# Kernel tuning notes

Hardware: AMD Instinct MI355X
Metric: run time of the kernel (lower is better)

## Reference

```python
import jax, jax.numpy as jnp
import numpy as np

HIDDEN_SIZE = 512  # H * d = 8 * 64


def setup_inputs() -> dict:
    key = jax.random.key(0)
    kq, kk, kv = jax.random.split(key, 3)
    B, H, S, d = 2, 8, 4096, 64
    Q = jax.random.normal(kq, (B, H, S, d), dtype=jnp.float32)
    K = jax.random.normal(kk, (B, H, d, S), dtype=jnp.float32)  # pre-transposed, as the torch module expects
    V = jax.random.normal(kv, (B, H, S, d), dtype=jnp.float32)
    return {"Q": Q, "K": K, "V": V}


def reference(Q, K, V):
    B, H, S, d = Q.shape
    scale = 1.0 / np.sqrt(HIDDEN_SIZE).astype(np.float32)
    # e: [B,H,S,S] -- full score matrix, as in the original
    e = jnp.einsum('bhsd,bhdt->bhst', Q, K) * scale
    # FAITHFUL quirk: nn.Softmax(dim=1) normalizes over the HEAD axis, not keys
    a = jax.nn.softmax(e, axis=1)
    o = jnp.einsum('bhst,bhtd->bhsd', a, V)
    # torch .view(B, S, hidden): raw contiguous reshape of [B,H,S,d]
    return o.reshape(B, S, HIDDEN_SIZE)
```

## Files before the change

### kernel.cpp

```cpp
#include <hip/hip_runtime.h>
#include <hip/hip_fp16.h>

#define S_LEN 4096
#define NHEAD 8
#define HEADD 64
#define BM 32
#define BN 32
#define TSPLIT 8
#define TCHUNK (S_LEN / TSPLIT)
#define NTILE (TCHUNK / BN)
#define EAP 48
#define KPRE 0.0637588696f

#define KT_BYTES (2ull * NHEAD * S_LEN * HEADD * 2)
#define VT_OFF   KT_BYTES
#define PART_OFF (2 * KT_BYTES)
#define PART_U32 (16ull * NHEAD * 2048 * 64)
#define WS_FULL  (PART_OFF + PART_U32 * 4)

typedef __attribute__((ext_vector_type(8))) short   short8;
typedef __attribute__((ext_vector_type(4))) float   float4v;

__device__ __forceinline__ unsigned short f2bf(float f) {
  unsigned int u = __float_as_uint(f);
  u += 0x7FFFu + ((u >> 16) & 1u);
  return (unsigned short)(u >> 16);
}
__device__ __forceinline__ float fast_exp2(float x) {
  float r; asm("v_exp_f32 %0, %1" : "=v"(r) : "v"(x)); return r;
}

__global__ __launch_bounds__(256)
void prepass_cvt(const float* __restrict__ K, const float* __restrict__ V,
                 unsigned short* __restrict__ Kt, unsigned short* __restrict__ Vt) {
  __shared__ __align__(16) unsigned short lds[64][72];
  const int tid = threadIdx.x;
  const int isV = blockIdx.x >> 10;
  const int idx = blockIdx.x & 1023;
  const int bh  = idx >> 6;
  const int t0  = (idx & 63) << 6;
  if (!isV) {
    const float* in = K + (size_t)bh * HEADD * S_LEN;
#pragma unroll
    for (int j = 0; j < 16; ++j) {
      int li = j * 256 + tid;
      int k = li >> 6, t = li & 63;
      lds[t][k] = f2bf(in[(size_t)k * S_LEN + t0 + t] * KPRE);
    }
    __syncthreads();
    unsigned short* out = Kt + (size_t)bh * S_LEN * HEADD;
    int t = tid >> 2, k0 = (tid & 3) << 4;
    *(short8*)(out + (size_t)(t0 + t) * HEADD + k0)     = *(const short8*)&lds[t][k0];
    *(short8*)(out + (size_t)(t0 + t) * HEADD + k0 + 8) = *(const short8*)&lds[t][k0 + 8];
  } else {
    const float* in = V + (size_t)bh * S_LEN * HEADD;
#pragma unroll
    for (int j = 0; j < 16; ++j) {
      int li = j * 256 + tid;
      int t = li >> 6, d = li & 63;
      lds[d][t] = f2bf(in[(size_t)(t0 + t) * HEADD + d]);
    }
    __syncthreads();
    unsigned short* out = Vt + (size_t)bh * HEADD * S_LEN;
    int d = tid >> 2, c0 = (tid & 3) << 4;
    *(short8*)(out + (size_t)d * S_LEN + t0 + c0)     = *(const short8*)&lds[d][c0];
    *(short8*)(out + (size_t)d * S_LEN + t0 + c0 + 8) = *(const short8*)&lds[d][c0 + 8];
  }
}

__global__ __launch_bounds__(512, 6)
void attn_main(const float* __restrict__ Q, const unsigned short* __restrict__ Kt,
               const unsigned short* __restrict__ Vt, unsigned int* __restrict__ part) {
  __shared__ __align__(16) unsigned short EA[2][NHEAD][BM][EAP];

  const int tid  = threadIdx.x;
  const int h    = tid >> 6;
  const int lane = tid & 63;
  const int quad = lane >> 4;
  const int l15  = lane & 15;
  const int combo = blockIdx.x & 15;
  const int b  = combo & 1;
  const int tc = combo >> 1;
  const int s0 = (blockIdx.x >> 4) * BM;

  const float* Qg = Q + (size_t)(b * NHEAD + h) * S_LEN * HEADD;
  const unsigned short* Kth = Kt + (size_t)(b * NHEAD + h) * S_LEN * HEADD;
  const unsigned short* Vth = Vt + (size_t)(b * NHEAD + h) * HEADD * S_LEN;

  short8 qf[2][2];
#pragma unroll
  for (int ss = 0; ss < 2; ++ss)
#pragma unroll
    for (int kk = 0; kk < 2; ++kk) {
      const float* p = Qg + (size_t)(s0 + ss * 16 + l15) * HEADD + kk * 32 + quad * 8;
      float4v a0 = *(const float4v*)p;
      float4v a1 = *(const float4v*)(p + 4);
      short8 f;
      f[0] = (short)f2bf(a0[0]); f[1] = (short)f2bf(a0[1]);
      f[2] = (short)f2bf(a0[2]); f[3] = (short)f2bf(a0[3]);
      f[4] = (short)f2bf(a1[0]); f[5] = (short)f2bf(a1[1]);
      f[6] = (short)f2bf(a1[2]); f[7] = (short)f2bf(a1[3]);
      qf[ss][kk] = f;
    }

  float4v acc[2][4];
#pragma unroll
  for (int ss = 0; ss < 2; ++ss)
#pragma unroll
    for (int df = 0; df < 4; ++df)
      acc[ss][df] = (float4v){0.f, 0.f, 0.f, 0.f};

  const int s_sm = tid >> 4;
  const int tp   = tid & 15;

  int t0 = tc * TCHUNK;
  for (int it = 0; it < NTILE; ++it, t0 += BN) {
    const int p = it & 1;

    {
      short8 kf[2][2];
#pragma unroll
      for (int ts = 0; ts < 2; ++ts)
#pragma unroll
        for (int kh = 0; kh < 2; ++kh)
          kf[ts][kh] = *(const short8*)(Kth + (size_t)(t0 + ts * 16 + l15) * HEADD + kh * 32 + quad * 8);
#pragma unroll
      for (int ss = 0; ss < 2; ++ss)
#pragma unroll
        for (int ts = 0; ts < 2; ++ts) {
          float4v e = (float4v){0.f, 0.f, 0.f, 0.f};
          e = __builtin_amdgcn_mfma_f32_16x16x32_bf16(qf[ss][0], kf[ts][0], e, 0, 0, 0);
          e = __builtin_amdgcn_mfma_f32_16x16x32_bf16(qf[ss][1], kf[ts][1], e, 0, 0, 0);
#pragma unroll
          for (int r = 0; r < 4; ++r)
            EA[p][h][ss * 16 + quad * 4 + r][ts * 16 + l15] =
                __half_as_ushort(__float2half(e[r]));
        }
    }
    __syncthreads();

    {
      unsigned int x[8];
#pragma unroll
      for (int hh = 0; hh < 8; ++hh)
        x[hh] = *(const unsigned int*)&EA[p][hh][s_sm][tp * 2];
      {
        float pe[8]; float sum = 0.f;
#pragma unroll
        for (int hh = 0; hh < 8; ++hh) {
          pe[hh] = fast_exp2(__half2float(__ushort_as_half((unsigned short)(x[hh] & 0xffffu))));
          sum += pe[hh];
        }
        float inv = __builtin_amdgcn_rcpf(sum);
#pragma unroll
        for (int hh = 0; hh < 8; ++hh) {
          unsigned int u = __float_as_uint(pe[hh] * inv) + 0x8000u;
          EA[p][hh][s_sm][tp * 2] = (unsigned short)(u >> 16);
        }
      }
      {
        float pe[8]; float sum = 0.f;
#pragma unroll
        for (int hh = 0; hh < 8; ++hh) {
          pe[hh] = fast_exp2(__half2float(__ushort_as_half((unsigned short)(x[hh] >> 16))));
          sum += pe[hh];
        }
        float inv = __builtin_amdgcn_rcpf(sum);
#pragma unroll
        for (int hh = 0; hh < 8; ++hh) {
          unsigned int u = __float_as_uint(pe[hh] * inv) + 0x8000u;
          EA[p][hh][s_sm][tp * 2 + 1] = (unsigned short)(u >> 16);
        }
      }
    }
    __syncthreads();

    {
      short8 vf[4];
#pragma unroll
      for (int df = 0; df < 4; ++df)
        vf[df] = *(const short8*)(Vth + (size_t)(df * 16 + l15) * S_LEN + t0 + quad * 8);
      short8 af[2];
#pragma unroll
      for (int ss = 0; ss < 2; ++ss)
        af[ss] = *(const short8*)&EA[p][h][ss * 16 + l15][quad * 8];
#pragma unroll
      for (int ss = 0; ss < 2; ++ss)
#pragma unroll
        for (int df = 0; df < 4; ++df)
          acc[ss][df] = __builtin_amdgcn_mfma_f32_16x16x32_bf16(af[ss], vf[df], acc[ss][df], 0, 0, 0);
    }
  }

  unsigned int* pb = part + ((size_t)(tc * 2 + b) * NHEAD + h) * (2048ull * 64);
  const int spb = (s0 >> 1) + quad * 2;
#pragma unroll
  for (int ss = 0; ss < 2; ++ss)
#pragma unroll
    for (int df = 0; df < 4; ++df)
#pragma unroll
      for (int rp = 0; rp < 2; ++rp) {
        unsigned int ulo = __float_as_uint(acc[ss][df][rp * 2])     + 0x8000u;
        unsigned int uhi = __float_as_uint(acc[ss][df][rp * 2 + 1]) + 0x8000u;
        unsigned int pk  = __builtin_amdgcn_perm(uhi, ulo, 0x07060302u);
        pb[(size_t)(spb + ss * 8 + rp) * 64 + df * 16 + l15] = pk;
      }
}

__global__ __launch_bounds__(256)
void reduce_partials(const unsigned int* __restrict__ part, float* __restrict__ out) {
  const size_t TCSTRIDE = 2097152;
  size_t i = ((size_t)blockIdx.x * 256 + threadIdx.x) * 4;
  if (i >= TCSTRIDE) return;
  float lo[4] = {0.f, 0.f, 0.f, 0.f}, hi[4] = {0.f, 0.f, 0.f, 0.f};
#pragma unroll
  for (int tc = 0; tc < 8; ++tc) {
    uint4 v = *(const uint4*)(part + tc * TCSTRIDE + i);
    lo[0] += __uint_as_float(v.x << 16); hi[0] += __uint_as_float(v.x & 0xffff0000u);
    lo[1] += __uint_as_float(v.y << 16); hi[1] += __uint_as_float(v.y & 0xffff0000u);
    lo[2] += __uint_as_float(v.z << 16); hi[2] += __uint_as_float(v.z & 0xffff0000u);
    lo[3] += __uint_as_float(v.w << 16); hi[3] += __uint_as_float(v.w & 0xffff0000u);
  }
  size_t bh = i >> 17;
  unsigned int r = (unsigned int)(i & 131071u);
  unsigned int sp = r >> 6, d = r & 63u;
  float* o = out + ((size_t)bh * S_LEN + 2 * sp) * HEADD + d;
  *(float4v*)o        = (float4v){lo[0], lo[1], lo[2], lo[3]};
  *(float4v*)(o + 64) = (float4v){hi[0], hi[1], hi[2], hi[3]};
}

__global__ __launch_bounds__(512, 2)
void attn_fallback(const float* __restrict__ Qg0, const float* __restrict__ Kg0,
                   const float* __restrict__ Vg0, float* __restrict__ Og0) {
  __shared__ __align__(16) unsigned short Klds[NHEAD][32][72];
  __shared__ __align__(16) unsigned short Vlds[NHEAD][HEADD][40];
  __shared__ __align__(16) unsigned short EA2[NHEAD][64][40];
  const int tid = threadIdx.x, h = tid >> 6, lane = tid & 63, quad = lane >> 4, l15 = lane & 15;
  const int b = blockIdx.x >> 6, s0 = (blockIdx.x & 63) * 64;
  const float* Qg = Qg0 + ((size_t)(b * NHEAD + h)) * S_LEN * HEADD;
  const float* Kg = Kg0 + ((size_t)(b * NHEAD + h)) * HEADD * S_LEN;
  const float* Vg = Vg0 + ((size_t)(b * NHEAD + h)) * S_LEN * HEADD;
  float* Og = Og0 + ((size_t)(b * NHEAD + h)) * S_LEN * HEADD;
  const float SC = 0.04419417382415922f;
  short8 qf[4][2];
#pragma unroll
  for (int ss = 0; ss < 4; ++ss)
#pragma unroll
    for (int kk = 0; kk < 2; ++kk) {
      const float* p = Qg + (size_t)(s0 + ss * 16 + l15) * HEADD + kk * 32 + quad * 8;
      float4v a0 = *(const float4v*)p; float4v a1 = *(const float4v*)(p + 4);
      short8 f;
      f[0] = (short)f2bf(a0[0]); f[1] = (short)f2bf(a0[1]); f[2] = (short)f2bf(a0[2]); f[3] = (short)f2bf(a0[3]);
      f[4] = (short)f2bf(a1[0]); f[5] = (short)f2bf(a1[1]); f[6] = (short)f2bf(a1[2]); f[7] = (short)f2bf(a1[3]);
      qf[ss][kk] = f;
    }
  float4v acc[4][4];
#pragma unroll
  for (int ss = 0; ss < 4; ++ss)
#pragma unroll
    for (int ds = 0; ds < 4; ++ds) acc[ss][ds] = (float4v){0.f, 0.f, 0.f, 0.f};
  const int koct = lane >> 3, kt4 = (lane & 7) * 4, vdq = lane & 15, vtg = lane >> 4;
  const int s_sm = tid >> 3, t4_sm = (tid & 7) * 4;
  for (int it = 0; it < S_LEN / 32; ++it) {
    const int t0 = it * 32;
    {
      float buf[8][4];
#pragma unroll
      for (int j = 0; j < 8; ++j) {
        float4v v = *(const float4v*)(Kg + (size_t)(koct * 8 + j) * S_LEN + t0 + kt4);
        buf[j][0] = v[0]; buf[j][1] = v[1]; buf[j][2] = v[2]; buf[j][3] = v[3];
      }
#pragma unroll
      for (int c = 0; c < 4; ++c) {
        short8 f;
#pragma unroll
        for (int j = 0; j < 8; ++j) f[j] = (short)f2bf(buf[j][c]);
        *(short8*)&Klds[h][kt4 + c][koct * 8] = f;
      }
    }
    {
      float buf[8][4];
#pragma unroll
      for (int j = 0; j < 8; ++j) {
        float4v v = *(const float4v*)(Vg + (size_t)(t0 + vtg * 8 + j) * HEADD + vdq * 4);
        buf[j][0] = v[0]; buf[j][1] = v[1]; buf[j][2] = v[2]; buf[j][3] = v[3];
      }
#pragma unroll
      for (int c = 0; c < 4; ++c) {
        short8 f;
#pragma unroll
        for (int j = 0; j < 8; ++j) f[j] = (short)f2bf(buf[j][c]);
        *(short8*)&Vlds[h][vdq * 4 + c][vtg * 8] = f;
      }
    }
    __syncthreads();
#pragma unroll
    for (int ts = 0; ts < 2; ++ts) {
      short8 kf0 = *(const short8*)&Klds[h][ts * 16 + l15][quad * 8];
      short8 kf1 = *(const short8*)&Klds[h][ts * 16 + l15][32 + quad * 8];
#pragma unroll
      for (int ss = 0; ss < 4; ++ss) {
        float4v e = (float4v){0.f, 0.f, 0.f, 0.f};
        e = __builtin_amdgcn_mfma_f32_16x16x32_bf16(qf[ss][0], kf0, e, 0, 0, 0);
        e = __builtin_amdgcn_mfma_f32_16x16x32_bf16(qf[ss][1], kf1, e, 0, 0, 0);
#pragma unroll
        for (int r = 0; r < 4; ++r)
          EA2[h][ss * 16 + quad * 4 + r][ts * 16 + l15] = __half_as_ushort(__float2half(e[r] * SC));
      }
    }
    __syncthreads();
    {
      float ev[8][4];
#pragma unroll
      for (int hh = 0; hh < 8; ++hh) {
        unsigned long long u = *(const unsigned long long*)&EA2[hh][s_sm][t4_sm];
        ev[hh][0] = __half2float(__ushort_as_half((unsigned short)u));
        ev[hh][1] = __half2float(__ushort_as_half((unsigned short)(u >> 16)));
        ev[hh][2] = __half2float(__ushort_as_half((unsigned short)(u >> 32)));
        ev[hh][3] = __half2float(__ushort_as_half((unsigned short)(u >> 48)));
      }
#pragma unroll
      for (int c = 0; c < 4; ++c) {
        float m = ev[0][c];
#pragma unroll
        for (int hh = 1; hh < 8; ++hh) m = fmaxf(m, ev[hh][c]);
        float sum = 0.f;
#pragma unroll
        for (int hh = 0; hh < 8; ++hh) { float x = __expf(ev[hh][c] - m); ev[hh][c] = x; sum += x; }
        float inv = __builtin_amdgcn_rcpf(sum);
#pragma unroll
        for (int hh = 0; hh < 8; ++hh) ev[hh][c] *= inv;
      }
#pragma unroll
      for (int hh = 0; hh < 8; ++hh) {
        unsigned short u0 = f2bf(ev[hh][0]), u1 = f2bf(ev[hh][1]), u2 = f2bf(ev[hh][2]), u3 = f2bf(ev[hh][3]);
        unsigned long long w = (unsigned long long)u0 | ((unsigned long long)u1 << 16) |
                               ((unsigned long long)u2 << 32) | ((unsigned long long)u3 << 48);
        *(unsigned long long*)&EA2[hh][s_sm][t4_sm] = w;
      }
    }
    __syncthreads();
    {
      short8 af[4], vf[4];
#pragma unroll
      for (int ss = 0; ss < 4; ++ss) af[ss] = *(const short8*)&EA2[h][ss * 16 + l15][quad * 8];
#pragma unroll
      for (int ds = 0; ds < 4; ++ds) vf[ds] = *(const short8*)&Vlds[h][ds * 16 + l15][quad * 8];
#pragma unroll
      for (int ss = 0; ss < 4; ++ss)
#pragma unroll
        for (int ds = 0; ds < 4; ++ds)
          acc[ss][ds] = __builtin_amdgcn_mfma_f32_16x16x32_bf16(af[ss], vf[ds], acc[ss][ds], 0, 0, 0);
    }
    __syncthreads();
  }
#pragma unroll
  for (int ss = 0; ss < 4; ++ss)
#pragma unroll
    for (int ds = 0; ds < 4; ++ds)
#pragma unroll
      for (int r = 0; r < 4; ++r)
        Og[(size_t)(s0 + ss * 16 + quad * 4 + r) * HEADD + ds * 16 + l15] = acc[ss][ds][r];
}

extern "C" void kernel_launch(void* const* d_in, const int* in_sizes, int n_in,
                              void* d_out, int out_size, void* d_ws, size_t ws_size,
                              hipStream_t stream) {
  const float* Q = (const float*)d_in[0];
  const float* K = (const float*)d_in[1];
  const float* V = (const float*)d_in[2];
  float* O = (float*)d_out;

  if (ws_size >= WS_FULL) {
    unsigned short* Kt = (unsigned short*)d_ws;
    unsigned short* Vt = (unsigned short*)((char*)d_ws + VT_OFF);
    unsigned int* part = (unsigned int*)((char*)d_ws + PART_OFF);
    hipLaunchKernelGGL(prepass_cvt, dim3(2048), dim3(256), 0, stream, K, V, Kt, Vt);
    hipLaunchKernelGGL(attn_main, dim3(2048), dim3(512), 0, stream, Q, Kt, Vt, part);
    hipLaunchKernelGGL(reduce_partials, dim3(2048), dim3(256), 0, stream, part, O);
  } else {
    hipLaunchKernelGGL(attn_fallback, dim3(128), dim3(512), 0, stream, Q, K, V, O);
  }
}
```

Baseline: 361.6 us.

## Fold exp into score stage and redundantly reduce head sums per warp

Each warp now applies exp2 to its own scores before writing fp16 values to LDS. After a single barrier, every warp reads all eight heads' exp values for its rows, sums them in half2, and normalizes its own head's values in registers. This removes the separate softmax pass and one __syncthreads per tile. The trade is eightfold redundant LDS reads and additions across warps, plus fp16 accumulation of the sum, which may lose precision. The LDS row padding also shrinks from 48 to 40.

```diff
diff --git a/kernel.cpp b/kernel.cpp
--- a/kernel.cpp
+++ b/kernel.cpp
@@ -1,5 +1,6 @@
 #include <hip/hip_runtime.h>
 #include <hip/hip_fp16.h>
+#include <cmath>
 
 #define S_LEN 4096
 #define NHEAD 8
@@ -9,7 +10,7 @@
 #define TSPLIT 8
 #define TCHUNK (S_LEN / TSPLIT)
 #define NTILE (TCHUNK / BN)
-#define EAP 48
+#define EAP 40
 #define KPRE 0.0637588696f
 
 #define KT_BYTES (2ull * NHEAD * S_LEN * HEADD * 2)
@@ -25,9 +26,6 @@
   unsigned int u = __float_as_uint(f);
   u += 0x7FFFu + ((u >> 16) & 1u);
   return (unsigned short)(u >> 16);
-}
-__device__ __forceinline__ float fast_exp2(float x) {
-  float r; asm("v_exp_f32 %0, %1" : "=v"(r) : "v"(x)); return r;
 }
 
 __global__ __launch_bounds__(256)
@@ -110,12 +108,11 @@
     for (int df = 0; df < 4; ++df)
       acc[ss][df] = (float4v){0.f, 0.f, 0.f, 0.f};
 
-  const int s_sm = tid >> 4;
-  const int tp   = tid & 15;
-
-  int t0 = tc * TCHUNK;
-  for (int it = 0; it < NTILE; ++it, t0 += BN) {
-    const int p = it & 1;
+  const int tbase = tc * TCHUNK;
+
+  for (int it = 0; it < NTILE; ++it) {
+    const int t0 = tbase + it * BN;
+    const int p  = it & 1;
 
     {
       short8 kf[2][2];
@@ -132,64 +129,51 @@
           e = __builtin_amdgcn_mfma_f32_16x16x32_bf16(qf[ss][0], kf[ts][0], e, 0, 0, 0);
           e = __builtin_amdgcn_mfma_f32_16x16x32_bf16(qf[ss][1], kf[ts][1], e, 0, 0, 0);
 #pragma unroll
-          for (int r = 0; r < 4; ++r)
+          for (int r = 0; r < 4; ++r) {
+            float ex = exp2f(e[r]);
             EA[p][h][ss * 16 + quad * 4 + r][ts * 16 + l15] =
-                __half_as_ushort(__float2half(e[r]));
+                __half_as_ushort(__float2half(ex));
+          }
         }
     }
     __syncthreads();
 
-    {
-      unsigned int x[8];
-#pragma unroll
-      for (int hh = 0; hh < 8; ++hh)
-        x[hh] = *(const unsigned int*)&EA[p][hh][s_sm][tp * 2];
-      {
-        float pe[8]; float sum = 0.f;
-#pragma unroll
-        for (int hh = 0; hh < 8; ++hh) {
-          pe[hh] = fast_exp2(__half2float(__ushort_as_half((unsigned short)(x[hh] & 0xffffu))));
-          sum += pe[hh];
-        }
-        float inv = __builtin_amdgcn_rcpf(sum);
-#pragma unroll
-        for (int hh = 0; hh < 8; ++hh) {
-          unsigned int u = __float_as_uint(pe[hh] * inv) + 0x8000u;
-          EA[p][hh][s_sm][tp * 2] = (unsigned short)(u >> 16);
-        }
-      }
-      {
-        float pe[8]; float sum = 0.f;
-#pragma unroll
-        for (int hh = 0; hh < 8; ++hh) {
-          pe[hh] = fast_exp2(__half2float(__ushort_as_half((unsigned short)(x[hh] >> 16))));
-          sum += pe[hh];
-        }
-        float inv = __builtin_amdgcn_rcpf(sum);
-#pragma unroll
-        for (int hh = 0; hh < 8; ++hh) {
-          unsigned int u = __float_as_uint(pe[hh] * inv) + 0x8000u;
-          EA[p][hh][s_sm][tp * 2 + 1] = (unsigned short)(u >> 16);
-        }
-      }
-    }
-    __syncthreads();
-
-    {
-      short8 vf[4];
+    short8 vf[4];
+#pragma unroll
+    for (int df = 0; df < 4; ++df)
+      vf[df] = *(const short8*)(Vth + (size_t)(df * 16 + l15) * S_LEN + t0 + quad * 8);
+
+    short8 af[2];
+#pragma unroll
+    for (int ss = 0; ss < 2; ++ss) {
+      const int row = ss * 16 + l15;
+      union { short8 s8; __half2 h2[4]; } w, own;
+      __half2 z[4];
+      w.s8 = *(const short8*)&EA[p][0][row][quad * 8];
+      z[0] = w.h2[0]; z[1] = w.h2[1]; z[2] = w.h2[2]; z[3] = w.h2[3];
+#pragma unroll
+      for (int hh = 1; hh < 8; ++hh) {
+        w.s8 = *(const short8*)&EA[p][hh][row][quad * 8];
+        z[0] = __hadd2(z[0], w.h2[0]); z[1] = __hadd2(z[1], w.h2[1]);
+        z[2] = __hadd2(z[2], w.h2[2]); z[3] = __hadd2(z[3], w.h2[3]);
+      }
+      own.s8 = *(const short8*)&EA[p][h][row][quad * 8];
+      short8 a8;
+#pragma unroll
+      for (int j = 0; j < 4; ++j) {
+        float il = __builtin_amdgcn_rcpf(__low2float(z[j]));
+        float ih = __builtin_amdgcn_rcpf(__high2float(z[j]));
+        a8[2 * j]     = (short)f2bf(__low2float(own.h2[j]) * il);
+        a8[2 * j + 1] = (short)f2bf(__high2float(own.h2[j]) * ih);
+      }
+      af[ss] = a8;
+    }
+
+#pragma unroll
+    for (int ss = 0; ss < 2; ++ss)
 #pragma unroll
       for (int df = 0; df < 4; ++df)
-        vf[df] = *(const short8*)(Vth + (size_t)(df * 16 + l15) * S_LEN + t0 + quad * 8);
-      short8 af[2];
-#pragma unroll
-      for (int ss = 0; ss < 2; ++ss)
-        af[ss] = *(const short8*)&EA[p][h][ss * 16 + l15][quad * 8];
-#pragma unroll
-      for (int ss = 0; ss < 2; ++ss)
-#pragma unroll
-        for (int df = 0; df < 4; ++df)
-          acc[ss][df] = __builtin_amdgcn_mfma_f32_16x16x32_bf16(af[ss], vf[df], acc[ss][df], 0, 0, 0);
-    }
+        acc[ss][df] = __builtin_amdgcn_mfma_f32_16x16x32_bf16(af[ss], vf[df], acc[ss][df], 0, 0, 0);
   }
 
   unsigned int* pb = part + ((size_t)(tc * 2 + b) * NHEAD + h) * (2048ull * 64);
```

Result: slower. 503.3 us (+39.2%).
